# Optimization experiments

Measured on AMD Instinct MI355X. Metric: run time of the kernel, lower is better.

Reference implementation:

```python
import jax, jax.numpy as jnp
import numpy as np

SR = 24000          # sampling_rate
MAX_H = 60          # min(n_harmonics=100, 60)


def _interp_linear(x, T):
    """Linear upsample along axis 1, align_corners=True. x: [B, C, F] -> [B, T, F]."""
    B, C, F = x.shape
    src = jnp.arange(T, dtype=x.dtype) * ((C - 1) / (T - 1))
    i0 = jnp.clip(jnp.floor(src).astype(jnp.int32), 0, C - 2)
    frac = (src - i0.astype(x.dtype))[None, :, None]
    return x[:, i0, :] * (1.0 - frac) + x[:, i0 + 1, :] * frac


def setup_inputs() -> dict:
    key = jax.random.key(0)
    k1, k2, k3, k4, k5 = jax.random.split(key, 5)
    B, T, H, C, NF = 8, 48000, MAX_H, 100, 5
    f0 = 100.0 + 300.0 * jax.random.uniform(k1, (B, T, 1), dtype=jnp.float32)
    amplitudes = jax.random.uniform(k2, (B, T, H), dtype=jnp.float32)
    formant_freqs = 200.0 + 3300.0 * jax.random.uniform(k3, (B, C, NF), dtype=jnp.float32)
    formant_bws = 50.0 + 150.0 * jax.random.uniform(k4, (B, C, NF), dtype=jnp.float32)
    formant_amps = jax.random.uniform(k5, (B, C, NF), dtype=jnp.float32)
    initial_phase = jnp.zeros((B, 1, 1), dtype=jnp.float32)
    return {"f0": f0, "amplitudes": amplitudes, "formant_freqs": formant_freqs,
            "formant_bws": formant_bws, "formant_amps": formant_amps,
            "initial_phase": initial_phase}


def reference(f0, amplitudes, formant_freqs, formant_bws, formant_amps, initial_phase):
    B, T, _ = f0.shape
    f0 = jax.lax.stop_gradient(f0)                    # torch: f0.detach()
    voiced = (f0[..., 0] > 0).astype(f0.dtype)        # [B, T]
    phase = jnp.cumsum(2.0 * np.pi * f0 / SR, axis=1) + initial_phase  # [B, T, 1]

    ff = _interp_linear(formant_freqs, T)             # [B, T, NF]
    fb = _interp_linear(formant_bws, T)
    fa = _interp_linear(formant_amps, T)

    h = jnp.arange(1, MAX_H + 1, dtype=f0.dtype)      # [H]
    h_freq = f0 * h                                   # [B, T, H]
    nyq = (h_freq < SR / 2).astype(f0.dtype)          # [B, T, H]

    # formant resonance factor: prod over formants of (1 + amp*bw^2/((h_freq-freq)^2+bw^2))
    factor = jnp.ones_like(h_freq)
    for f in range(ff.shape[-1]):                     # NF = 5, small fixed loop
        freq = ff[:, :, f:f + 1]
        bw = fb[:, :, f:f + 1]
        amp = fa[:, :, f:f + 1]
        factor = factor * (1.0 + amp * bw * bw / ((h_freq - freq) ** 2 + bw * bw))

    osc = jnp.sin(phase * h)                          # [B, T, H]
    signal = jnp.sum(osc * amplitudes * factor * nyq, axis=-1) * voiced  # [B, T]

    final_phase = jax.lax.stop_gradient(phase[:, -1:, :] % (2.0 * np.pi))  # [B, 1, 1]
    return signal, final_phase
```

## Files before the change

kernel.cpp:

```cpp
#include <hip/hip_runtime.h>
#include <math.h>

#define SRATE   24000.0
#define NB      8
#define NT      48000
#define NH      60
#define NC      100
#define NFMT    5
#define CTS     64
#define NCH     (NT / CTS)
#define TWO_PI  6.283185307179586476925286766559
#define PSC     (1.0f / 1024.0f)
#define NYQS    11.71875f

typedef float v2f __attribute__((ext_vector_type(2)));

__global__ __launch_bounds__(256) void k_partial(const float* __restrict__ f0,
                                                 double* __restrict__ part) {
    int b = blockIdx.y;
    int ch = blockIdx.x * 4 + (threadIdx.x >> 6);
    int lane = threadIdx.x & 63;
    if (ch < NCH) {
        int t = ch * CTS + lane;
        double q = (double)f0[b * NT + t];
        #pragma unroll
        for (int off = 32; off > 0; off >>= 1)
            q += __shfl_down(q, off, 64);
        if (lane == 0) part[b * NCH + ch] = q;
    }
}

__global__ __launch_bounds__(256) void k_main(const float* __restrict__ f0,
                                              const float* __restrict__ amps,
                                              const float* __restrict__ ffq,
                                              const float* __restrict__ fbw,
                                              const float* __restrict__ fam,
                                              const float* __restrict__ initp,
                                              const double* __restrict__ part,
                                              float* __restrict__ out) {
    int b = blockIdx.y;
    int ch = blockIdx.x * 4 + (threadIdx.x >> 6);
    int lane = threadIdx.x & 63;
    if (ch >= NCH) return;
    int t0 = ch * CTS;
    int g0 = lane >> 2, j = lane & 3;
    const float4 f4z = make_float4(0.f, 0.f, 0.f, 0.f);
    const float* ab = amps + (size_t)b * NT * NH;

    #define AMPLD(S0, S1, S2, S3, p)                                          \
        { const float4* rr =                                                  \
              (const float4*)(ab + (size_t)(t0 + (p) * 16 + g0) * NH);        \
          S0 = rr[j]; S1 = rr[4 + j]; S2 = rr[8 + j];                         \
          S3 = (j < 3) ? rr[12 + j] : f4z; }

    float4 A0, A1, A2, A3, B0, B1, B2, B3;
    AMPLD(A0, A1, A2, A3, 0)
    AMPLD(B0, B1, B2, B3, 1)

    const double* pb = part + b * NCH;
    double sl = 0.0;
    #pragma unroll
    for (int k = 0; k < 12; ++k) {
        int idx = k * 64 + lane;
        double v = (idx < NCH) ? pb[idx] : 0.0;
        if (idx < ch) sl += v;
    }
    #pragma unroll
    for (int off = 1; off < 64; off <<= 1)
        sl += __shfl_xor(sl, off, 64);

    double initrev = (double)initp[b] * (1.0 / TWO_PI);

    if (ch == 0) {
        double sa = 0.0;
        #pragma unroll
        for (int k = 0; k < 12; ++k) {
            int idx = k * 64 + lane;
            if (idx < NCH) sa += pb[idx];
        }
        #pragma unroll
        for (int off = 1; off < 64; off <<= 1)
            sa += __shfl_xor(sa, off, 64);
        if (lane == 0) {
            double rv = sa * (1.0 / SRATE) + initrev;
            out[NB * NT + b] = (float)((rv - floor(rv)) * TWO_PI);
        }
    }

    double pfrac = sl * (1.0 / SRATE) + initrev;
    float prefF = (float)(pfrac - floor(pfrac));

    float f0v = f0[b * NT + t0 + lane];
    float incf = f0v;
    #pragma unroll
    for (int off = 1; off < 64; off <<= 1) {
        float n = __shfl_up(incf, off, 64);
        if (lane >= off) incf += n;
    }
    float rev_l = __builtin_amdgcn_fractf(prefF + incf * (1.0f / 24000.0f));
    float f0s_l = f0v * PSC;

    double srcd = (double)(t0 + lane) * (99.0 / 47999.0);
    int i0 = (int)srcd;
    if (i0 > NC - 2) i0 = NC - 2;
    float frac = (float)(srcd - (double)i0);
    float omf = 1.0f - frac;
    const float* Fq = ffq + (b * NC + i0) * NFMT;
    const float* Bw = fbw + (b * NC + i0) * NFMT;
    const float* Am = fam + (b * NC + i0) * NFMT;
    float fqs[NFMT], c1s[NFMT], c2s[NFMT];
    #pragma unroll
    for (int f = 0; f < NFMT; ++f) {
        float fqv = Fq[f] * omf + Fq[NFMT + f] * frac;
        float bwv = Bw[f] * omf + Bw[NFMT + f] * frac;
        float amv = Am[f] * omf + Am[NFMT + f] * frac;
        float bws = bwv * PSC;
        fqs[f] = fqv * PSC;
        c2s[f] = bws * bws;
        c1s[f] = amv * c2s[f];
    }

    auto do_pass = [&](int p, float4 q0, float4 q1, float4 q2, float4 q3) {
        int gp = (p << 4) + g0;
        float f0s   = __shfl(f0s_l, gp, 64);
        float rev_g = __shfl(rev_l, gp, 64);
        float fq[NFMT], c1[NFMT], c2[NFMT];
        #pragma unroll
        for (int f = 0; f < NFMT; ++f) {
            fq[f] = __shfl(fqs[f], gp, 64);
            c1[f] = __shfl(c1s[f], gp, 64);
            c2[f] = __shfl(c2s[f], gp, 64);
        }
        float hb = (float)(j << 2);
        auto sd = [&](float k) {
            return __builtin_amdgcn_sinf(
                __builtin_amdgcn_fractf((hb + k) * rev_g));
        };
        v2f s01 = {sd(1.0f),  sd(2.0f)};
        v2f s23 = {sd(3.0f),  sd(4.0f)};
        v2f s45 = {sd(17.0f), sd(18.0f)};
        v2f s67 = {sd(19.0f), sd(20.0f)};
        float c16 = __builtin_amdgcn_cosf(
            __builtin_amdgcn_fractf(16.0f * rev_g));
        v2f cv = {2.0f * c16, 2.0f * c16};
        v2f s89 = cv * s45 - s01;
        v2f sAB = cv * s67 - s23;
        v2f sCD = cv * s89 - s45;
        v2f sEF = cv * sAB - s67;
        v2f acc2 = {0.0f, 0.0f};
        auto pairf = [&](float h1, v2f sn, float a0, float a1) {
            v2f hfl = {h1, h1 + 1.0f};
            v2f hs = f0s * hfl;
            v2f pN = {1.0f, 1.0f}, pD = {1.0f, 1.0f};
            #pragma unroll
            for (int f = 0; f < NFMT; ++f) {
                v2f d = hs - fq[f];
                v2f e = d * d + c2[f];
                pN *= e + c1[f];
                pD *= e;
            }
            float R = __builtin_amdgcn_rcpf(pD.x * pD.y);
            v2f fac = {pN.x * pD.y * R, pN.y * pD.x * R};
            v2f fm;
            fm.x = (hs.x < NYQS) ? fac.x : 0.0f;
            fm.y = (hs.y < NYQS) ? fac.y : 0.0f;
            v2f aa = {a0, a1};
            acc2 += (sn * aa) * fm;
        };
        pairf(hb + 1.0f,  s01, q0.x, q0.y);
        pairf(hb + 3.0f,  s23, q0.z, q0.w);
        pairf(hb + 17.0f, s45, q1.x, q1.y);
        pairf(hb + 19.0f, s67, q1.z, q1.w);
        pairf(hb + 33.0f, s89, q2.x, q2.y);
        pairf(hb + 35.0f, sAB, q2.z, q2.w);
        pairf(hb + 49.0f, sCD, q3.x, q3.y);
        pairf(hb + 51.0f, sEF, q3.z, q3.w);
        float acc = acc2.x + acc2.y;
        acc += __shfl_xor(acc, 1, 64);
        acc += __shfl_xor(acc, 2, 64);
        if (j == 0) {
            if (!(f0s > 0.0f)) acc = 0.0f;
            out[b * NT + t0 + (p << 4) + g0] = acc;
        }
    };

    do_pass(0, A0, A1, A2, A3);
    AMPLD(A0, A1, A2, A3, 2)
    do_pass(1, B0, B1, B2, B3);
    AMPLD(B0, B1, B2, B3, 3)
    do_pass(2, A0, A1, A2, A3);
    do_pass(3, B0, B1, B2, B3);
    #undef AMPLD
}

extern "C" void kernel_launch(void* const* d_in, const int* in_sizes, int n_in,
                              void* d_out, int out_size, void* d_ws, size_t ws_size,
                              hipStream_t stream) {
    const float* f0    = (const float*)d_in[0];
    const float* amps  = (const float*)d_in[1];
    const float* ffq   = (const float*)d_in[2];
    const float* fbw   = (const float*)d_in[3];
    const float* fam   = (const float*)d_in[4];
    const float* initp = (const float*)d_in[5];
    float* out = (float*)d_out;

    double* part = (double*)d_ws;

    dim3 gchunk((NCH + 3) / 4, NB);
    k_partial<<<gchunk, 256, 0, stream>>>(f0, part);
    k_main<<<gchunk, 256, 0, stream>>>(f0, amps, ffq, fbw, fam, initp, part, out);
}
```

Before: 32.85 us.

## Stage amplitude tile into LDS via async global_load_lds with one-wave blocks

Each block is now a single wavefront handling one 64-sample chunk. At kernel entry the whole 64x60 amplitude tile is issued as asynchronous global-to-LDS loads, while the prefix sums, formant interpolation and phase scan run, instead of double-buffering amplitudes in registers. Prefix and total sums are merged into one pass over preloaded partials. The aim is to hide memory latency and cut register pressure. The costs are 15 KB of LDS per wave, a full vmcnt(0) wait before compute, and possible LDS bank conflicts on the 60-float row stride.

```diff
diff --git a/kernel.cpp b/kernel.cpp
--- a/kernel.cpp
+++ b/kernel.cpp
@@ -30,75 +30,30 @@
     }
 }
 
-__global__ __launch_bounds__(256) void k_main(const float* __restrict__ f0,
-                                              const float* __restrict__ amps,
-                                              const float* __restrict__ ffq,
-                                              const float* __restrict__ fbw,
-                                              const float* __restrict__ fam,
-                                              const float* __restrict__ initp,
-                                              const double* __restrict__ part,
-                                              float* __restrict__ out) {
+__global__ __launch_bounds__(64) void k_main(const float* __restrict__ f0,
+                                             const float* __restrict__ amps,
+                                             const float* __restrict__ ffq,
+                                             const float* __restrict__ fbw,
+                                             const float* __restrict__ fam,
+                                             const float* __restrict__ initp,
+                                             const double* __restrict__ part,
+                                             float* __restrict__ out) {
     int b = blockIdx.y;
-    int ch = blockIdx.x * 4 + (threadIdx.x >> 6);
-    int lane = threadIdx.x & 63;
-    if (ch >= NCH) return;
+    int ch = blockIdx.x;
+    int lane = threadIdx.x;
     int t0 = ch * CTS;
     int g0 = lane >> 2, j = lane & 3;
-    const float4 f4z = make_float4(0.f, 0.f, 0.f, 0.f);
-    const float* ab = amps + (size_t)b * NT * NH;
-
-    #define AMPLD(S0, S1, S2, S3, p)                                          \
-        { const float4* rr =                                                  \
-              (const float4*)(ab + (size_t)(t0 + (p) * 16 + g0) * NH);        \
-          S0 = rr[j]; S1 = rr[4 + j]; S2 = rr[8 + j];                         \
-          S3 = (j < 3) ? rr[12 + j] : f4z; }
-
-    float4 A0, A1, A2, A3, B0, B1, B2, B3;
-    AMPLD(A0, A1, A2, A3, 0)
-    AMPLD(B0, B1, B2, B3, 1)
+
+    __shared__ float smem[CTS * 60];
 
     const double* pb = part + b * NCH;
-    double sl = 0.0;
+    double pv[12];
     #pragma unroll
     for (int k = 0; k < 12; ++k) {
         int idx = k * 64 + lane;
-        double v = (idx < NCH) ? pb[idx] : 0.0;
-        if (idx < ch) sl += v;
-    }
-    #pragma unroll
-    for (int off = 1; off < 64; off <<= 1)
-        sl += __shfl_xor(sl, off, 64);
-
-    double initrev = (double)initp[b] * (1.0 / TWO_PI);
-
-    if (ch == 0) {
-        double sa = 0.0;
-        #pragma unroll
-        for (int k = 0; k < 12; ++k) {
-            int idx = k * 64 + lane;
-            if (idx < NCH) sa += pb[idx];
-        }
-        #pragma unroll
-        for (int off = 1; off < 64; off <<= 1)
-            sa += __shfl_xor(sa, off, 64);
-        if (lane == 0) {
-            double rv = sa * (1.0 / SRATE) + initrev;
-            out[NB * NT + b] = (float)((rv - floor(rv)) * TWO_PI);
-        }
-    }
-
-    double pfrac = sl * (1.0 / SRATE) + initrev;
-    float prefF = (float)(pfrac - floor(pfrac));
-
+        pv[k] = (idx < NCH) ? pb[idx] : 0.0;
+    }
     float f0v = f0[b * NT + t0 + lane];
-    float incf = f0v;
-    #pragma unroll
-    for (int off = 1; off < 64; off <<= 1) {
-        float n = __shfl_up(incf, off, 64);
-        if (lane >= off) incf += n;
-    }
-    float rev_l = __builtin_amdgcn_fractf(prefF + incf * (1.0f / 24000.0f));
-    float f0s_l = f0v * PSC;
 
     double srcd = (double)(t0 + lane) * (99.0 / 47999.0);
     int i0 = (int)srcd;
@@ -108,19 +63,71 @@
     const float* Fq = ffq + (b * NC + i0) * NFMT;
     const float* Bw = fbw + (b * NC + i0) * NFMT;
     const float* Am = fam + (b * NC + i0) * NFMT;
+    float tq[10];
+    #pragma unroll
+    for (int f = 0; f < NFMT; ++f) { tq[f] = Fq[f]; tq[5 + f] = Fq[NFMT + f]; }
+    float tb[10];
+    #pragma unroll
+    for (int f = 0; f < NFMT; ++f) { tb[f] = Bw[f]; tb[5 + f] = Bw[NFMT + f]; }
+    float ta[10];
+    #pragma unroll
+    for (int f = 0; f < NFMT; ++f) { ta[f] = Am[f]; ta[5 + f] = Am[NFMT + f]; }
+
+    const float* gsrc = amps + (size_t)b * NT * NH + (size_t)t0 * NH;
+    #pragma unroll
+    for (int i = 0; i < 15; ++i) {
+        __builtin_amdgcn_global_load_lds(
+            (const __attribute__((address_space(1))) void*)(gsrc + i * 256 + lane * 4),
+            (__attribute__((address_space(3))) void*)(&smem[i * 256]),
+            16, 0, 0);
+    }
+
+    double sl = 0.0, sa = 0.0;
+    #pragma unroll
+    for (int k = 0; k < 12; ++k) {
+        int idx = k * 64 + lane;
+        sa += pv[k];
+        if (idx < ch) sl += pv[k];
+    }
+    #pragma unroll
+    for (int off = 1; off < 64; off <<= 1) {
+        sl += __shfl_xor(sl, off, 64);
+        sa += __shfl_xor(sa, off, 64);
+    }
+    double initrev = (double)initp[b] * (1.0 / TWO_PI);
+    if (ch == 0 && lane == 0) {
+        double rv = sa * (1.0 / SRATE) + initrev;
+        out[NB * NT + b] = (float)((rv - floor(rv)) * TWO_PI);
+    }
+
+    double pfrac = sl * (1.0 / SRATE) + initrev;
+    float prefF = (float)(pfrac - floor(pfrac));
+
+    float incf = f0v;
+    #pragma unroll
+    for (int off = 1; off < 64; off <<= 1) {
+        float n = __shfl_up(incf, off, 64);
+        if (lane >= off) incf += n;
+    }
+    float rev_l = __builtin_amdgcn_fractf(prefF + incf * (1.0f / 24000.0f));
+    float f0s_l = f0v * PSC;
+
     float fqs[NFMT], c1s[NFMT], c2s[NFMT];
     #pragma unroll
     for (int f = 0; f < NFMT; ++f) {
-        float fqv = Fq[f] * omf + Fq[NFMT + f] * frac;
-        float bwv = Bw[f] * omf + Bw[NFMT + f] * frac;
-        float amv = Am[f] * omf + Am[NFMT + f] * frac;
+        float fqv = tq[f] * omf + tq[5 + f] * frac;
+        float bwv = tb[f] * omf + tb[5 + f] * frac;
+        float amv = ta[f] * omf + ta[5 + f] * frac;
         float bws = bwv * PSC;
         fqs[f] = fqv * PSC;
         c2s[f] = bws * bws;
         c1s[f] = amv * c2s[f];
     }
 
-    auto do_pass = [&](int p, float4 q0, float4 q1, float4 q2, float4 q3) {
+    asm volatile("s_waitcnt vmcnt(0)" ::: "memory");
+    __builtin_amdgcn_sched_barrier(0);
+
+    auto do_pass = [&](int p) {
         int gp = (p << 4) + g0;
         float f0s   = __shfl(f0s_l, gp, 64);
         float rev_g = __shfl(rev_l, gp, 64);
@@ -131,6 +138,12 @@
             c1[f] = __shfl(c1s[f], gp, 64);
             c2[f] = __shfl(c2s[f], gp, 64);
         }
+        const float4* rowp = (const float4*)&smem[gp * 60];
+        float4 q0 = rowp[j];
+        float4 q1 = rowp[4 + j];
+        float4 q2 = rowp[8 + j];
+        float4 q3 = (j < 3) ? rowp[12 + j]
+                            : make_float4(0.f, 0.f, 0.f, 0.f);
         float hb = (float)(j << 2);
         auto sd = [&](float k) {
             return __builtin_amdgcn_sinf(
@@ -184,13 +197,10 @@
         }
     };
 
-    do_pass(0, A0, A1, A2, A3);
-    AMPLD(A0, A1, A2, A3, 2)
-    do_pass(1, B0, B1, B2, B3);
-    AMPLD(B0, B1, B2, B3, 3)
-    do_pass(2, A0, A1, A2, A3);
-    do_pass(3, B0, B1, B2, B3);
-    #undef AMPLD
+    do_pass(0);
+    do_pass(1);
+    do_pass(2);
+    do_pass(3);
 }
 
 extern "C" void kernel_launch(void* const* d_in, const int* in_sizes, int n_in,
@@ -206,7 +216,8 @@
 
     double* part = (double*)d_ws;
 
-    dim3 gchunk((NCH + 3) / 4, NB);
-    k_partial<<<gchunk, 256, 0, stream>>>(f0, part);
-    k_main<<<gchunk, 256, 0, stream>>>(f0, amps, ffq, fbw, fam, initp, part, out);
+    dim3 gpart((NCH + 3) / 4, NB);
+    k_partial<<<gpart, 256, 0, stream>>>(f0, part);
+    dim3 gmain(NCH, NB);
+    k_main<<<gmain, 64, 0, stream>>>(f0, amps, ffq, fbw, fam, initp, part, out);
 }
```

Measured after the change: 37.25 us. +13.4%, slower.
